# Kernel tuning notes

Hardware: AMD Instinct MI355X
Metric: run time of the kernel (lower is better)

## Reference

```python
import jax, jax.numpy as jnp
import numpy as np

N, E, D_IN, H = 40000, 640000, 128, 128
R, B = 8, 30  # num_relations = 2*n_speakers**2, num_bases


def setup_inputs() -> dict:
    key = jax.random.key(0)
    ks = jax.random.split(key, 10)
    node_features = jax.random.normal(ks[0], (N, D_IN), jnp.float32)
    edge_index = jax.random.randint(ks[1], (2, E), 0, N)
    edge_type = jax.random.randint(ks[2], (E,), 0, R)
    edge_norm = jax.random.uniform(ks[3], (E,), jnp.float32)
    s_in = 1.0 / np.sqrt(D_IN)
    s_h = 1.0 / np.sqrt(H)
    basis = jax.random.normal(ks[4], (B, D_IN, H), jnp.float32) * s_in
    comp = jax.random.normal(ks[5], (R, B), jnp.float32) * (1.0 / np.sqrt(B))
    root = jax.random.normal(ks[6], (D_IN, H), jnp.float32) * s_in
    bias1 = jnp.zeros((H,), jnp.float32)
    w_rel = jax.random.normal(ks[7], (H, H), jnp.float32) * s_h
    w_root2 = jax.random.normal(ks[8], (H, H), jnp.float32) * s_h
    bias2 = jnp.zeros((H,), jnp.float32)
    return dict(node_features=node_features, edge_index=edge_index,
                edge_norm=edge_norm, edge_type=edge_type,
                basis=basis, comp=comp, root=root, bias1=bias1,
                w_rel=w_rel, w_root2=w_root2, bias2=bias2)


def reference(node_features, edge_index, edge_norm, edge_type,
              basis, comp, root, bias1, w_rel, w_root2, bias2):
    n = node_features.shape[0]
    src, dst = edge_index[0], edge_index[1]  # messages flow src -> dst

    # ---- RGCNConv (basis decomposition, mean aggregation, root + bias) ----
    # Per-relation weights from bases: [R, D_in, H]
    w = jnp.einsum('rb,bio->rio', comp, basis)
    # Transform all nodes by every relation once (avoids per-edge matmul): [R, N, H]
    xw = jnp.einsum('nd,rdo->rno', node_features, w)
    msgs = xw[edge_type, src]                                  # [E, H]
    agg = jax.ops.segment_sum(msgs, dst, num_segments=n)       # [N, H]
    deg = jax.ops.segment_sum(jnp.ones_like(dst, dtype=node_features.dtype),
                              dst, num_segments=n)
    agg = agg / jnp.maximum(deg, 1.0)[:, None]                 # mean aggregation
    h = agg + node_features @ root + bias1                     # [N, H]

    # ---- GraphConv (add aggregation): W_rel * sum_j x_j + W_root * x_i + b ----
    nbr = jax.ops.segment_sum(h[src], dst, num_segments=n)     # [N, H]
    out = nbr @ w_rel + h @ w_root2 + bias2
    return out
```

## Files before the change

### kernel.cpp

```cpp
#include <hip/hip_runtime.h>
#include <stdint.h>

#define DH 128
#define NB 30
#define NR 8

typedef short bf16x8 __attribute__((ext_vector_type(8)));
typedef float f32x4 __attribute__((ext_vector_type(4)));
typedef float f32x2 __attribute__((ext_vector_type(2)));

static __device__ __forceinline__ unsigned short f2bf(float f) {
    unsigned u = __float_as_uint(f);
    u += 0x7fffu + ((u >> 16) & 1u);
    return (unsigned short)(u >> 16);
}
static __device__ __forceinline__ float bflo(unsigned u) { return __uint_as_float(u << 16); }
static __device__ __forceinline__ float bfhi(unsigned u) { return __uint_as_float(u & 0xffff0000u); }


__global__ __launch_bounds__(256) void k_prephist(const float* __restrict__ comp,
                                                  const float* __restrict__ basis,
                                                  const float* __restrict__ root,
                                                  const float* __restrict__ wrel,
                                                  const float* __restrict__ wroot2,
                                                  unsigned short* __restrict__ wallT,
                                                  unsigned short* __restrict__ WT2,
                                                  const int* __restrict__ dstA, int E,
                                                  int* __restrict__ deg,
                                                  int* __restrict__ rank, int histB) {
    int b = blockIdx.x;
    int tid = threadIdx.x;
    if (b < histB) {
        int e = b * 256 + tid;
        if (e < E) rank[e] = atomicAdd(&deg[dstA[e]], 1);
        return;
    }
    int unit = (b - histB) * 2 + (tid >> 7);
    int o = tid & 127;
    int i = unit & 127;
    int y = unit >> 7;
    if (y < NR) {
        float s = 0.f;
        #pragma unroll
        for (int bb = 0; bb < NB; ++bb)
            s += comp[y * NB + bb] * basis[((size_t)bb * DH + i) * DH + o];
        wallT[((size_t)y * DH + o) * DH + i] = f2bf(s);
    } else if (y == NR) {
        wallT[((size_t)NR * DH + o) * DH + i] = f2bf(root[i * DH + o]);
    } else {
        const float* W = (y == NR + 2) ? wroot2 : wrel;
        int id = (i & 7) * 16 + (i >> 3);
        WT2[((size_t)(y - NR - 1) * DH + o) * DH + i] = f2bf(W[(size_t)id * DH + o]);
    }
}

__global__ __launch_bounds__(1024) void k_scan(const int* __restrict__ deg, int n, int total_n,
                                               int* __restrict__ offsets,
                                               unsigned long long* __restrict__ st,
                                               int* __restrict__ ticket) {
    __shared__ int s[1024];
    __shared__ int bid_s, pre_s;
    const int tid = threadIdx.x;
    if (tid == 0) bid_s = atomicAdd(ticket, 1);
    __syncthreads();
    const int b = bid_s;
    const int base = b * 4096 + tid * 4;
    int v[4];
    #pragma unroll
    for (int j = 0; j < 4; ++j) {
        int i = base + j;
        v[j] = (i < n) ? deg[i] : 0;
    }
    int tsum = v[0] + v[1] + v[2] + v[3];
    s[tid] = tsum;
    __syncthreads();
    for (int off = 1; off < 1024; off <<= 1) {
        int t = (tid >= off) ? s[tid - off] : 0;
        __syncthreads();
        s[tid] += t;
        __syncthreads();
    }
    if (tid == 0) {
        int total = s[1023];
        atomicExch(&st[b], (1ULL << 62) | (unsigned long long)(unsigned)total);
        long long pre = 0;
        int t = b - 1;
        while (t >= 0) {
            unsigned long long w;
            do { w = atomicAdd(&st[t], 0ULL); } while (w == 0ULL);
            pre += (long long)(w & 0x3FFFFFFFFFFFFFFFULL);
            if ((w >> 62) == 2ULL) break;
            --t;
        }
        atomicExch(&st[b], (2ULL << 62) | (unsigned long long)(pre + total));
        pre_s = (int)pre;
    }
    __syncthreads();
    int run = pre_s + s[tid] - tsum;
    #pragma unroll
    for (int j = 0; j < 4; ++j) {
        int i = base + j;
        if (i < total_n) offsets[i] = run;
        run += v[j];
    }
}

__global__ __launch_bounds__(512, 4) void k_gemm1s(const float* __restrict__ x,
                                                   const unsigned short* __restrict__ wallT,
                                                   const float* __restrict__ bias1,
                                                   int Nn,
                                                   unsigned* __restrict__ xw8,
                                                   unsigned short* __restrict__ hb,
                                                   const int* __restrict__ src,
                                                   const int* __restrict__ dstA,
                                                   const int* __restrict__ etype, int E,
                                                   const int* __restrict__ offsets,
                                                   const int* __restrict__ rank,
                                                   unsigned* __restrict__ sorted,
                                                   int scatB, int gx) {
    __shared__ __align__(16) unsigned short As[128][136];
    __shared__ __align__(16) unsigned short Bs[128][136];
    const int tid = threadIdx.x;
    const int b = blockIdx.x;

    const bool is_scat = (b < 2 * scatB) && (b & 1);

    if (is_scat) {
        const int sidx = b >> 1;
        const int stride = scatB * 512;
        for (int e = sidx * 512 + tid; e < E; e += stride) {
            int d = dstA[e];
            int pos = offsets[d] + rank[e];
            sorted[pos] = (unsigned)src[e] | ((unsigned)etype[e] << 17);
        }
        return;
    }

    const int bg = (b < 2 * scatB) ? (b >> 1) : (b - scatB);
    const int wave = tid >> 6, lane = tid & 63;
    const int g = bg / gx;
    const int rowbase = (bg % gx) * 128;
    const int lq = lane >> 4, lr = lane & 15;

    #pragma unroll
    for (int it = 0; it < 4; ++it) {
        int c = it * 512 + tid;
        int row = c >> 4, col = c & 15;
        int rg = rowbase + row; if (rg >= Nn) rg = Nn - 1;
        float4 v0 = *(const float4*)&x[(size_t)rg * DH + col * 8];
        float4 v1 = *(const float4*)&x[(size_t)rg * DH + col * 8 + 4];
        uint4 u;
        u.x = (unsigned)f2bf(v0.x) | ((unsigned)f2bf(v0.y) << 16);
        u.y = (unsigned)f2bf(v0.z) | ((unsigned)f2bf(v0.w) << 16);
        u.z = (unsigned)f2bf(v1.x) | ((unsigned)f2bf(v1.y) << 16);
        u.w = (unsigned)f2bf(v1.z) | ((unsigned)f2bf(v1.w) << 16);
        *(uint4*)&As[row][col * 8] = u;
    }

    for (int rr = 0; rr < 3; ++rr) {
        const int r = g * 3 + rr;
        const unsigned short* WT = wallT + (size_t)r * DH * DH;
        if (rr) __syncthreads();
        #pragma unroll
        for (int it = 0; it < 4; ++it) {
            int c = it * 512 + tid;
            int row = c >> 4, col = c & 15;
            *(uint4*)&Bs[row][col * 8] = *(const uint4*)&WT[(size_t)row * DH + col * 8];
        }
        __syncthreads();

        f32x4 acc[8];
        #pragma unroll
        for (int nt = 0; nt < 8; ++nt) acc[nt] = (f32x4)0.f;

        #pragma unroll
        for (int ks = 0; ks < 4; ++ks) {
            const int ko = ks * 32 + lq * 8;
            bf16x8 a0 = *(const bf16x8*)&As[wave * 16 + lr][ko];
            #pragma unroll
            for (int nt = 0; nt < 8; ++nt) {
                bf16x8 bb = *(const bf16x8*)&Bs[nt * 16 + lr][ko];
                acc[nt] = __builtin_amdgcn_mfma_f32_16x16x32_bf16(a0, bb, acc[nt], 0, 0, 0);
            }
        }
        if (r < NR) {
            unsigned* dst = xw8 + ((size_t)r * Nn + rowbase) * (DH / 4);
            #pragma unroll
            for (int reg = 0; reg < 4; ++reg) {
                int m = wave * 16 + lq * 4 + reg;
                if (rowbase + m < Nn) {
                    uint2 o;
                    o.x = __builtin_amdgcn_cvt_pk_fp8_f32(acc[0][reg], acc[1][reg], 0, false);
                    o.x = __builtin_amdgcn_cvt_pk_fp8_f32(acc[2][reg], acc[3][reg], o.x, true);
                    o.y = __builtin_amdgcn_cvt_pk_fp8_f32(acc[4][reg], acc[5][reg], 0, false);
                    o.y = __builtin_amdgcn_cvt_pk_fp8_f32(acc[6][reg], acc[7][reg], o.y, true);
                    *(uint2*)&dst[(size_t)m * (DH / 4) + lr * 2] = o;
                }
            }
        } else {
            float bv[8];
            #pragma unroll
            for (int nt = 0; nt < 8; ++nt) bv[nt] = bias1[nt * 16 + lr];
            #pragma unroll
            for (int reg = 0; reg < 4; ++reg) {
                int m = rowbase + wave * 16 + lq * 4 + reg;
                if (m < Nn) {
                    uint4 u;
                    u.x = (unsigned)f2bf(acc[0][reg] + bv[0]) | ((unsigned)f2bf(acc[1][reg] + bv[1]) << 16);
                    u.y = (unsigned)f2bf(acc[2][reg] + bv[2]) | ((unsigned)f2bf(acc[3][reg] + bv[3]) << 16);
                    u.z = (unsigned)f2bf(acc[4][reg] + bv[4]) | ((unsigned)f2bf(acc[5][reg] + bv[5]) << 16);
                    u.w = (unsigned)f2bf(acc[6][reg] + bv[6]) | ((unsigned)f2bf(acc[7][reg] + bv[7]) << 16);
                    *(uint4*)&hb[(size_t)m * DH + lr * 8] = u;
                }
            }
        }
    }
}

__global__ __launch_bounds__(256) void k_agg1(const int* __restrict__ offsets,
                                              const unsigned* __restrict__ sorted,
                                              const unsigned* __restrict__ xw8,
                                              const unsigned* __restrict__ hb32,
                                              int Nn, unsigned* __restrict__ hbf) {
    int w = (blockIdx.x * blockDim.x + threadIdx.x) >> 6;
    if (w >= Nn) return;
    int lane = threadIdx.x & 63;
    int half = lane >> 5, sub = lane & 31;
    int s = offsets[w], e = offsets[w + 1];
    float a0 = 0.f, a1 = 0.f, a2 = 0.f, a3 = 0.f;
    int p = s;
    for (; p + 16 <= e; p += 16) {
        unsigned pk[8];
        #pragma unroll
        for (int j = 0; j < 8; ++j) pk[j] = sorted[p + 2 * j + half];
        unsigned u[8];
        #pragma unroll
        for (int j = 0; j < 8; ++j)
            u[j] = xw8[((size_t)(pk[j] >> 17) * Nn + (pk[j] & 0x1FFFFu)) * 32 + sub];
        #pragma unroll
        for (int j = 0; j < 8; ++j) {
            f32x2 lo = __builtin_amdgcn_cvt_pk_f32_fp8(u[j], false);
            f32x2 hi = __builtin_amdgcn_cvt_pk_f32_fp8(u[j], true);
            a0 += lo.x; a1 += lo.y; a2 += hi.x; a3 += hi.y;
        }
    }
    if (p < e) {
        unsigned pk[8]; float m[8];
        #pragma unroll
        for (int j = 0; j < 8; ++j) {
            int q = p + 2 * j + half; bool v = q < e;
            pk[j] = sorted[v ? q : e - 1];
            m[j] = v ? 1.f : 0.f;
        }
        unsigned u[8];
        #pragma unroll
        for (int j = 0; j < 8; ++j)
            u[j] = xw8[((size_t)(pk[j] >> 17) * Nn + (pk[j] & 0x1FFFFu)) * 32 + sub];
        #pragma unroll
        for (int j = 0; j < 8; ++j) {
            f32x2 lo = __builtin_amdgcn_cvt_pk_f32_fp8(u[j], false);
            f32x2 hi = __builtin_amdgcn_cvt_pk_f32_fp8(u[j], true);
            a0 = fmaf(m[j], lo.x, a0);
            a1 = fmaf(m[j], lo.y, a1);
            a2 = fmaf(m[j], hi.x, a2);
            a3 = fmaf(m[j], hi.y, a3);
        }
    }
    a0 += __shfl_xor(a0, 32, 64);
    a1 += __shfl_xor(a1, 32, 64);
    a2 += __shfl_xor(a2, 32, 64);
    a3 += __shfl_xor(a3, 32, 64);
    if (half == 0) {
        float invd = 1.0f / fmaxf((float)(e - s), 1.0f);
        uint2 hv = *(const uint2*)&hb32[(size_t)w * 64 + sub * 2];
        float h0 = bflo(hv.x) + a0 * invd;
        float h1 = bfhi(hv.x) + a1 * invd;
        float h2 = bflo(hv.y) + a2 * invd;
        float h3 = bfhi(hv.y) + a3 * invd;
        uint2 o;
        o.x = (unsigned)f2bf(h0) | ((unsigned)f2bf(h1) << 16);
        o.y = (unsigned)f2bf(h2) | ((unsigned)f2bf(h3) << 16);
        *(uint2*)&hbf[(size_t)w * 64 + sub * 2] = o;
    }
}

__global__ __launch_bounds__(512, 4) void k_gemm2d(const unsigned short* __restrict__ hbf,
                                                   const unsigned short* __restrict__ WT2,
                                                   const float* __restrict__ bias2,
                                                   int Nn,
                                                   unsigned short* __restrict__ hw,
                                                   unsigned short* __restrict__ hro) {
    __shared__ __align__(16) unsigned short As[128][136];
    __shared__ __align__(16) unsigned short Bs[128][136];
    const int tid = threadIdx.x;
    const int wave = tid >> 6, lane = tid & 63;
    const int rowbase = blockIdx.x * 128;
    const int lq = lane >> 4, lr = lane & 15;

    #pragma unroll
    for (int it = 0; it < 4; ++it) {
        int c = it * 512 + tid;
        int row = c >> 4, col = c & 15;
        int rg = rowbase + row; if (rg >= Nn) rg = Nn - 1;
        *(uint4*)&As[row][col * 8] = *(const uint4*)&hbf[(size_t)rg * DH + col * 8];
    }

    for (int ph = 0; ph < 2; ++ph) {
        const unsigned short* WT = WT2 + (size_t)ph * DH * DH;
        if (ph) __syncthreads();
        #pragma unroll
        for (int it = 0; it < 4; ++it) {
            int c = it * 512 + tid;
            int row = c >> 4, col = c & 15;
            *(uint4*)&Bs[row][col * 8] = *(const uint4*)&WT[(size_t)row * DH + col * 8];
        }
        __syncthreads();

        f32x4 acc[8];
        #pragma unroll
        for (int nt = 0; nt < 8; ++nt) acc[nt] = (f32x4)0.f;

        #pragma unroll
        for (int ks = 0; ks < 4; ++ks) {
            const int ko = ks * 32 + lq * 8;
            bf16x8 a0 = *(const bf16x8*)&As[wave * 16 + lr][ko];
            #pragma unroll
            for (int nt = 0; nt < 8; ++nt) {
                bf16x8 bb = *(const bf16x8*)&Bs[nt * 16 + lr][ko];
                acc[nt] = __builtin_amdgcn_mfma_f32_16x16x32_bf16(a0, bb, acc[nt], 0, 0, 0);
            }
        }

        unsigned short* dst = ph ? hro : hw;
        float bv[8];
        #pragma unroll
        for (int nt = 0; nt < 8; ++nt) bv[nt] = ph ? bias2[nt * 16 + lr] : 0.f;
        #pragma unroll
        for (int reg = 0; reg < 4; ++reg) {
            int m = rowbase + wave * 16 + lq * 4 + reg;
            if (m < Nn) {
                uint4 u;
                u.x = (unsigned)f2bf(acc[0][reg] + bv[0]) | ((unsigned)f2bf(acc[1][reg] + bv[1]) << 16);
                u.y = (unsigned)f2bf(acc[2][reg] + bv[2]) | ((unsigned)f2bf(acc[3][reg] + bv[3]) << 16);
                u.z = (unsigned)f2bf(acc[4][reg] + bv[4]) | ((unsigned)f2bf(acc[5][reg] + bv[5]) << 16);
                u.w = (unsigned)f2bf(acc[6][reg] + bv[6]) | ((unsigned)f2bf(acc[7][reg] + bv[7]) << 16);
                *(uint4*)&dst[(size_t)m * DH + lr * 8] = u;
            }
        }
    }
}

__global__ __launch_bounds__(256) void k_aggout(const int* __restrict__ offsets,
                                                const unsigned* __restrict__ sorted,
                                                const uint2* __restrict__ hw2,
                                                const unsigned* __restrict__ hro32,
                                                int Nn, float* __restrict__ out) {
    int w = (blockIdx.x * blockDim.x + threadIdx.x) >> 6;
    if (w >= Nn) return;
    int lane = threadIdx.x & 63;
    int half = lane >> 5, sub = lane & 31;
    int s = offsets[w], e = offsets[w + 1];
    float a0 = 0.f, a1 = 0.f, a2 = 0.f, a3 = 0.f;
    int p = s;
    for (; p + 16 <= e; p += 16) {
        unsigned pk[8];
        #pragma unroll
        for (int j = 0; j < 8; ++j) pk[j] = sorted[p + 2 * j + half];
        uint2 u[8];
        #pragma unroll
        for (int j = 0; j < 8; ++j)
            u[j] = hw2[(size_t)(pk[j] & 0x1FFFFu) * 32 + sub];
        #pragma unroll
        for (int j = 0; j < 8; ++j) {
            a0 += bflo(u[j].x); a1 += bfhi(u[j].x);
            a2 += bflo(u[j].y); a3 += bfhi(u[j].y);
        }
    }
    if (p < e) {
        unsigned pk[8]; float m[8];
        #pragma unroll
        for (int j = 0; j < 8; ++j) {
            int q = p + 2 * j + half; bool v = q < e;
            pk[j] = sorted[v ? q : e - 1];
            m[j] = v ? 1.f : 0.f;
        }
        uint2 u[8];
        #pragma unroll
        for (int j = 0; j < 8; ++j)
            u[j] = hw2[(size_t)(pk[j] & 0x1FFFFu) * 32 + sub];
        #pragma unroll
        for (int j = 0; j < 8; ++j) {
            a0 = fmaf(m[j], bflo(u[j].x), a0);
            a1 = fmaf(m[j], bfhi(u[j].x), a1);
            a2 = fmaf(m[j], bflo(u[j].y), a2);
            a3 = fmaf(m[j], bfhi(u[j].y), a3);
        }
    }
    a0 += __shfl_xor(a0, 32, 64);
    a1 += __shfl_xor(a1, 32, 64);
    a2 += __shfl_xor(a2, 32, 64);
    a3 += __shfl_xor(a3, 32, 64);
    if (half == 0) {
        uint2 hv = *(const uint2*)&hro32[(size_t)w * 64 + sub * 2];
        float rv[4];
        rv[0] = a0 + bflo(hv.x);
        rv[1] = a1 + bfhi(hv.x);
        rv[2] = a2 + bflo(hv.y);
        rv[3] = a3 + bfhi(hv.y);
        float* orow = &out[(size_t)w * DH];
        #pragma unroll
        for (int j = 0; j < 4; ++j) {
            int pp = sub * 4 + j;
            orow[(pp & 7) * 16 + (pp >> 3)] = rv[j];
        }
    }
}

extern "C" void kernel_launch(void* const* d_in, const int* in_sizes, int n_in,
                              void* d_out, int out_size, void* d_ws, size_t ws_size,
                              hipStream_t stream) {
    const float* x      = (const float*)d_in[0];
    const int*   eidx   = (const int*)d_in[1];
    const int*   etype  = (const int*)d_in[3];
    const float* basis  = (const float*)d_in[4];
    const float* comp   = (const float*)d_in[5];
    const float* root   = (const float*)d_in[6];
    const float* bias1  = (const float*)d_in[7];
    const float* wrel   = (const float*)d_in[8];
    const float* wroot2 = (const float*)d_in[9];
    const float* bias2  = (const float*)d_in[10];
    float* out = (float*)d_out;

    const int N = in_sizes[0] / DH;
    const int E = in_sizes[3];
    const int* srcA = eidx;
    const int* dstA = eidx + E;

    char* ws = (char*)d_ws;
    size_t off = 0;
    auto alloc = [&](size_t bytes) -> void* {
        void* p = (void*)(ws + off);
        off += (bytes + 255) & ~(size_t)255;
        return p;
    };
    int* deg           = (int*)alloc((size_t)N * 4);
    unsigned long long* st = (unsigned long long*)alloc(64 * 8);
    int* ticket        = (int*)alloc(256);
    int* rank          = (int*)alloc((size_t)E * 4);
    int* offsets       = (int*)alloc((size_t)(N + 1) * 4);
    unsigned* sorted   = (unsigned*)alloc((size_t)E * 4);
    unsigned short* wallT = (unsigned short*)alloc((size_t)(NR + 1) * DH * DH * 2);
    unsigned short* WT2   = (unsigned short*)alloc((size_t)2 * DH * DH * 2);
    unsigned* xw8      = (unsigned*)alloc((size_t)NR * N * DH);
    unsigned short* hb = (unsigned short*)alloc((size_t)N * DH * 2);
    unsigned* hbf      = (unsigned*)alloc((size_t)N * (DH / 2) * 4);
    unsigned short* hw  = (unsigned short*)alloc((size_t)N * DH * 2);
    unsigned short* hro = (unsigned short*)alloc((size_t)N * DH * 2);
    (void)ws_size; (void)n_in; (void)out_size;

    hipMemsetAsync(deg, 0, (size_t)N * 4 + 768, stream);

    const int histB = (E + 255) / 256;
    k_prephist<<<histB + 704, 256, 0, stream>>>(comp, basis, root, wrel, wroot2,
                                                wallT, WT2, dstA, E, deg, rank, histB);

    const int totn = N + 1;
    const int nsb = (totn + 4095) / 4096;
    k_scan<<<nsb, 1024, 0, stream>>>(deg, N, totn, offsets, st, ticket);

    const int gx = (N + 127) / 128;
    const int gemmB = gx * 3;
    const int scatB = 640;
    k_gemm1s<<<scatB + gemmB, 512, 0, stream>>>(x, wallT, bias1, N, xw8, hb,
                                                srcA, dstA, etype, E, offsets, rank, sorted,
                                                scatB, gx);

    k_agg1<<<(N * 64) / 256, 256, 0, stream>>>(offsets, sorted, xw8,
                                               (const unsigned*)hb, N, hbf);
    k_gemm2d<<<gx, 512, 0, stream>>>((const unsigned short*)hbf, WT2, bias2, N, hw, hro);
    k_aggout<<<(N * 64) / 256, 256, 0, stream>>>(offsets, sorted, (const uint2*)hw,
                                                 (const unsigned*)hro, N, out);
}
```

Before: 221.0 us.

## Fuse relation aggregation into second-layer GEMM via shared-memory tile

Merges the mean-aggregation kernel with the two H×H GEMMs. Each 512-thread block gathers fp8 messages for its 128 rows and writes the resulting h rows straight into the shared A tile, with no hbf buffer in global memory. This removes one launch and the write and re-read of the N×H bf16 intermediate. The cost is parallelism: the gather now runs on only gx blocks, each wave looping serially over 16 rows, instead of one wave per node, so latency hiding for the random gathers may suffer.

```diff
diff --git a/kernel.cpp b/kernel.cpp
--- a/kernel.cpp
+++ b/kernel.cpp
@@ -217,135 +217,155 @@
     }
 }
 
-__global__ __launch_bounds__(256) void k_agg1(const int* __restrict__ offsets,
-                                              const unsigned* __restrict__ sorted,
-                                              const unsigned* __restrict__ xw8,
-                                              const unsigned* __restrict__ hb32,
-                                              int Nn, unsigned* __restrict__ hbf) {
-    int w = (blockIdx.x * blockDim.x + threadIdx.x) >> 6;
-    if (w >= Nn) return;
-    int lane = threadIdx.x & 63;
-    int half = lane >> 5, sub = lane & 31;
-    int s = offsets[w], e = offsets[w + 1];
-    float a0 = 0.f, a1 = 0.f, a2 = 0.f, a3 = 0.f;
-    int p = s;
-    for (; p + 16 <= e; p += 16) {
-        unsigned pk[8];
-        #pragma unroll
-        for (int j = 0; j < 8; ++j) pk[j] = sorted[p + 2 * j + half];
-        unsigned u[8];
-        #pragma unroll
-        for (int j = 0; j < 8; ++j)
-            u[j] = xw8[((size_t)(pk[j] >> 17) * Nn + (pk[j] & 0x1FFFFu)) * 32 + sub];
-        #pragma unroll
-        for (int j = 0; j < 8; ++j) {
-            f32x2 lo = __builtin_amdgcn_cvt_pk_f32_fp8(u[j], false);
-            f32x2 hi = __builtin_amdgcn_cvt_pk_f32_fp8(u[j], true);
-            a0 += lo.x; a1 += lo.y; a2 += hi.x; a3 += hi.y;
-        }
-    }
-    if (p < e) {
-        unsigned pk[8]; float m[8];
-        #pragma unroll
-        for (int j = 0; j < 8; ++j) {
-            int q = p + 2 * j + half; bool v = q < e;
-            pk[j] = sorted[v ? q : e - 1];
-            m[j] = v ? 1.f : 0.f;
-        }
-        unsigned u[8];
-        #pragma unroll
-        for (int j = 0; j < 8; ++j)
-            u[j] = xw8[((size_t)(pk[j] >> 17) * Nn + (pk[j] & 0x1FFFFu)) * 32 + sub];
-        #pragma unroll
-        for (int j = 0; j < 8; ++j) {
-            f32x2 lo = __builtin_amdgcn_cvt_pk_f32_fp8(u[j], false);
-            f32x2 hi = __builtin_amdgcn_cvt_pk_f32_fp8(u[j], true);
-            a0 = fmaf(m[j], lo.x, a0);
-            a1 = fmaf(m[j], lo.y, a1);
-            a2 = fmaf(m[j], hi.x, a2);
-            a3 = fmaf(m[j], hi.y, a3);
-        }
-    }
-    a0 += __shfl_xor(a0, 32, 64);
-    a1 += __shfl_xor(a1, 32, 64);
-    a2 += __shfl_xor(a2, 32, 64);
-    a3 += __shfl_xor(a3, 32, 64);
-    if (half == 0) {
-        float invd = 1.0f / fmaxf((float)(e - s), 1.0f);
-        uint2 hv = *(const uint2*)&hb32[(size_t)w * 64 + sub * 2];
-        float h0 = bflo(hv.x) + a0 * invd;
-        float h1 = bfhi(hv.x) + a1 * invd;
-        float h2 = bflo(hv.y) + a2 * invd;
-        float h3 = bfhi(hv.y) + a3 * invd;
-        uint2 o;
-        o.x = (unsigned)f2bf(h0) | ((unsigned)f2bf(h1) << 16);
-        o.y = (unsigned)f2bf(h2) | ((unsigned)f2bf(h3) << 16);
-        *(uint2*)&hbf[(size_t)w * 64 + sub * 2] = o;
-    }
-}
-
-__global__ __launch_bounds__(512, 4) void k_gemm2d(const unsigned short* __restrict__ hbf,
-                                                   const unsigned short* __restrict__ WT2,
-                                                   const float* __restrict__ bias2,
-                                                   int Nn,
-                                                   unsigned short* __restrict__ hw,
-                                                   unsigned short* __restrict__ hro) {
+__global__ __launch_bounds__(512, 4) void k_aggemm2(const int* __restrict__ offsets,
+                                                    const unsigned* __restrict__ sorted,
+                                                    const unsigned* __restrict__ xw8,
+                                                    const unsigned* __restrict__ hb32,
+                                                    const unsigned short* __restrict__ WT2,
+                                                    const float* __restrict__ bias2,
+                                                    int Nn,
+                                                    unsigned short* __restrict__ hw,
+                                                    unsigned short* __restrict__ hro) {
     __shared__ __align__(16) unsigned short As[128][136];
     __shared__ __align__(16) unsigned short Bs[128][136];
     const int tid = threadIdx.x;
     const int wave = tid >> 6, lane = tid & 63;
     const int rowbase = blockIdx.x * 128;
     const int lq = lane >> 4, lr = lane & 15;
+    const int half = lane >> 5, sub = lane & 31;
 
     #pragma unroll
     for (int it = 0; it < 4; ++it) {
         int c = it * 512 + tid;
-        int row = c >> 4, col = c & 15;
-        int rg = rowbase + row; if (rg >= Nn) rg = Nn - 1;
-        *(uint4*)&As[row][col * 8] = *(const uint4*)&hbf[(size_t)rg * DH + col * 8];
-    }
-
-    for (int ph = 0; ph < 2; ++ph) {
-        const unsigned short* WT = WT2 + (size_t)ph * DH * DH;
-        if (ph) __syncthreads();
-        #pragma unroll
-        for (int it = 0; it < 4; ++it) {
-            int c = it * 512 + tid;
-            int row = c >> 4, col = c & 15;
-            *(uint4*)&Bs[row][col * 8] = *(const uint4*)&WT[(size_t)row * DH + col * 8];
-        }
-        __syncthreads();
-
-        f32x4 acc[8];
-        #pragma unroll
-        for (int nt = 0; nt < 8; ++nt) acc[nt] = (f32x4)0.f;
-
-        #pragma unroll
-        for (int ks = 0; ks < 4; ++ks) {
-            const int ko = ks * 32 + lq * 8;
-            bf16x8 a0 = *(const bf16x8*)&As[wave * 16 + lr][ko];
-            #pragma unroll
-            for (int nt = 0; nt < 8; ++nt) {
-                bf16x8 bb = *(const bf16x8*)&Bs[nt * 16 + lr][ko];
-                acc[nt] = __builtin_amdgcn_mfma_f32_16x16x32_bf16(a0, bb, acc[nt], 0, 0, 0);
+        *(uint4*)&Bs[c >> 4][(c & 15) * 8] = *(const uint4*)&WT2[(size_t)(c >> 4) * DH + (c & 15) * 8];
+    }
+
+    for (int i = 0; i < 16; ++i) {
+        int lrow = wave * 16 + i;
+        int w = rowbase + lrow;
+        if (w >= Nn) {
+            if (half == 0) *(uint2*)&As[lrow][sub * 4] = make_uint2(0u, 0u);
+            continue;
+        }
+        int s = offsets[w], e = offsets[w + 1];
+        float a0 = 0.f, a1 = 0.f, a2 = 0.f, a3 = 0.f;
+        int p = s;
+        for (; p + 16 <= e; p += 16) {
+            unsigned pk[8];
+            #pragma unroll
+            for (int j = 0; j < 8; ++j) pk[j] = sorted[p + 2 * j + half];
+            unsigned u[8];
+            #pragma unroll
+            for (int j = 0; j < 8; ++j)
+                u[j] = xw8[((size_t)(pk[j] >> 17) * Nn + (pk[j] & 0x1FFFFu)) * 32 + sub];
+            #pragma unroll
+            for (int j = 0; j < 8; ++j) {
+                f32x2 lo = __builtin_amdgcn_cvt_pk_f32_fp8(u[j], false);
+                f32x2 hi = __builtin_amdgcn_cvt_pk_f32_fp8(u[j], true);
+                a0 += lo.x; a1 += lo.y; a2 += hi.x; a3 += hi.y;
             }
         }
-
-        unsigned short* dst = ph ? hro : hw;
-        float bv[8];
-        #pragma unroll
-        for (int nt = 0; nt < 8; ++nt) bv[nt] = ph ? bias2[nt * 16 + lr] : 0.f;
-        #pragma unroll
-        for (int reg = 0; reg < 4; ++reg) {
-            int m = rowbase + wave * 16 + lq * 4 + reg;
-            if (m < Nn) {
-                uint4 u;
-                u.x = (unsigned)f2bf(acc[0][reg] + bv[0]) | ((unsigned)f2bf(acc[1][reg] + bv[1]) << 16);
-                u.y = (unsigned)f2bf(acc[2][reg] + bv[2]) | ((unsigned)f2bf(acc[3][reg] + bv[3]) << 16);
-                u.z = (unsigned)f2bf(acc[4][reg] + bv[4]) | ((unsigned)f2bf(acc[5][reg] + bv[5]) << 16);
-                u.w = (unsigned)f2bf(acc[6][reg] + bv[6]) | ((unsigned)f2bf(acc[7][reg] + bv[7]) << 16);
-                *(uint4*)&dst[(size_t)m * DH + lr * 8] = u;
+        if (p < e) {
+            unsigned pk[8]; float m[8];
+            #pragma unroll
+            for (int j = 0; j < 8; ++j) {
+                int q = p + 2 * j + half; bool v = q < e;
+                pk[j] = sorted[v ? q : e - 1];
+                m[j] = v ? 1.f : 0.f;
             }
+            unsigned u[8];
+            #pragma unroll
+            for (int j = 0; j < 8; ++j)
+                u[j] = xw8[((size_t)(pk[j] >> 17) * Nn + (pk[j] & 0x1FFFFu)) * 32 + sub];
+            #pragma unroll
+            for (int j = 0; j < 8; ++j) {
+                f32x2 lo = __builtin_amdgcn_cvt_pk_f32_fp8(u[j], false);
+                f32x2 hi = __builtin_amdgcn_cvt_pk_f32_fp8(u[j], true);
+                a0 = fmaf(m[j], lo.x, a0);
+                a1 = fmaf(m[j], lo.y, a1);
+                a2 = fmaf(m[j], hi.x, a2);
+                a3 = fmaf(m[j], hi.y, a3);
+            }
+        }
+        a0 += __shfl_xor(a0, 32, 64);
+        a1 += __shfl_xor(a1, 32, 64);
+        a2 += __shfl_xor(a2, 32, 64);
+        a3 += __shfl_xor(a3, 32, 64);
+        if (half == 0) {
+            float invd = 1.0f / fmaxf((float)(e - s), 1.0f);
+            uint2 hv = *(const uint2*)&hb32[(size_t)w * 64 + sub * 2];
+            float h0 = bflo(hv.x) + a0 * invd;
+            float h1 = bfhi(hv.x) + a1 * invd;
+            float h2 = bflo(hv.y) + a2 * invd;
+            float h3 = bfhi(hv.y) + a3 * invd;
+            uint2 o;
+            o.x = (unsigned)f2bf(h0) | ((unsigned)f2bf(h1) << 16);
+            o.y = (unsigned)f2bf(h2) | ((unsigned)f2bf(h3) << 16);
+            *(uint2*)&As[lrow][sub * 4] = o;
+        }
+    }
+    __syncthreads();
+
+    f32x4 acc[8];
+    #pragma unroll
+    for (int nt = 0; nt < 8; ++nt) acc[nt] = (f32x4)0.f;
+    #pragma unroll
+    for (int ks = 0; ks < 4; ++ks) {
+        const int ko = ks * 32 + lq * 8;
+        bf16x8 a0 = *(const bf16x8*)&As[wave * 16 + lr][ko];
+        #pragma unroll
+        for (int nt = 0; nt < 8; ++nt) {
+            bf16x8 bb = *(const bf16x8*)&Bs[nt * 16 + lr][ko];
+            acc[nt] = __builtin_amdgcn_mfma_f32_16x16x32_bf16(a0, bb, acc[nt], 0, 0, 0);
+        }
+    }
+    __syncthreads();
+
+    const unsigned short* WT1 = WT2 + (size_t)DH * DH;
+    #pragma unroll
+    for (int it = 0; it < 4; ++it) {
+        int c = it * 512 + tid;
+        *(uint4*)&Bs[c >> 4][(c & 15) * 8] = *(const uint4*)&WT1[(size_t)(c >> 4) * DH + (c & 15) * 8];
+    }
+    #pragma unroll
+    for (int reg = 0; reg < 4; ++reg) {
+        int m = rowbase + wave * 16 + lq * 4 + reg;
+        if (m < Nn) {
+            uint4 u;
+            u.x = (unsigned)f2bf(acc[0][reg]) | ((unsigned)f2bf(acc[1][reg]) << 16);
+            u.y = (unsigned)f2bf(acc[2][reg]) | ((unsigned)f2bf(acc[3][reg]) << 16);
+            u.z = (unsigned)f2bf(acc[4][reg]) | ((unsigned)f2bf(acc[5][reg]) << 16);
+            u.w = (unsigned)f2bf(acc[6][reg]) | ((unsigned)f2bf(acc[7][reg]) << 16);
+            *(uint4*)&hw[(size_t)m * DH + lr * 8] = u;
+        }
+    }
+    __syncthreads();
+
+    #pragma unroll
+    for (int nt = 0; nt < 8; ++nt) acc[nt] = (f32x4)0.f;
+    #pragma unroll
+    for (int ks = 0; ks < 4; ++ks) {
+        const int ko = ks * 32 + lq * 8;
+        bf16x8 a0 = *(const bf16x8*)&As[wave * 16 + lr][ko];
+        #pragma unroll
+        for (int nt = 0; nt < 8; ++nt) {
+            bf16x8 bb = *(const bf16x8*)&Bs[nt * 16 + lr][ko];
+            acc[nt] = __builtin_amdgcn_mfma_f32_16x16x32_bf16(a0, bb, acc[nt], 0, 0, 0);
+        }
+    }
+    float bv[8];
+    #pragma unroll
+    for (int nt = 0; nt < 8; ++nt) bv[nt] = bias2[nt * 16 + lr];
+    #pragma unroll
+    for (int reg = 0; reg < 4; ++reg) {
+        int m = rowbase + wave * 16 + lq * 4 + reg;
+        if (m < Nn) {
+            uint4 u;
+            u.x = (unsigned)f2bf(acc[0][reg] + bv[0]) | ((unsigned)f2bf(acc[1][reg] + bv[1]) << 16);
+            u.y = (unsigned)f2bf(acc[2][reg] + bv[2]) | ((unsigned)f2bf(acc[3][reg] + bv[3]) << 16);
+            u.z = (unsigned)f2bf(acc[4][reg] + bv[4]) | ((unsigned)f2bf(acc[5][reg] + bv[5]) << 16);
+            u.w = (unsigned)f2bf(acc[6][reg] + bv[6]) | ((unsigned)f2bf(acc[7][reg] + bv[7]) << 16);
+            *(uint4*)&hro[(size_t)m * DH + lr * 8] = u;
         }
     }
 }
@@ -453,7 +473,6 @@
     unsigned short* WT2   = (unsigned short*)alloc((size_t)2 * DH * DH * 2);
     unsigned* xw8      = (unsigned*)alloc((size_t)NR * N * DH);
     unsigned short* hb = (unsigned short*)alloc((size_t)N * DH * 2);
-    unsigned* hbf      = (unsigned*)alloc((size_t)N * (DH / 2) * 4);
     unsigned short* hw  = (unsigned short*)alloc((size_t)N * DH * 2);
     unsigned short* hro = (unsigned short*)alloc((size_t)N * DH * 2);
     (void)ws_size; (void)n_in; (void)out_size;
@@ -475,9 +494,8 @@
                                                 srcA, dstA, etype, E, offsets, rank, sorted,
                                                 scatB, gx);
 
-    k_agg1<<<(N * 64) / 256, 256, 0, stream>>>(offsets, sorted, xw8,
-                                               (const unsigned*)hb, N, hbf);
-    k_gemm2d<<<gx, 512, 0, stream>>>((const unsigned short*)hbf, WT2, bias2, N, hw, hro);
+    k_aggemm2<<<gx, 512, 0, stream>>>(offsets, sorted, xw8, (const unsigned*)hb,
+                                      WT2, bias2, N, hw, hro);
     k_aggout<<<(N * 64) / 256, 256, 0, stream>>>(offsets, sorted, (const uint2*)hw,
                                                  (const unsigned*)hro, N, out);
 }
```

Result: slower. 235.2 us (+6.4%).
